# Kernel tuning notes

Hardware: AMD Instinct MI355X
Metric: run time of the kernel (lower is better)

The kernel has to match this reference:

```python
import jax, jax.numpy as jnp
import numpy as np

B, N, C = 16, 1024, 1152
H = 16
D = C // H  # 72
INNER = 4608
EPS = 1e-6


def _layernorm(x, g, b):
    mu = jnp.mean(x, axis=-1, keepdims=True)
    var = jnp.mean(jnp.square(x - mu), axis=-1, keepdims=True)
    return (x - mu) * jax.lax.rsqrt(var + EPS) * g + b


def setup_inputs() -> dict:
    key = jax.random.key(0)
    ks = jax.random.split(key, 16)
    s_c = 1.0 / np.sqrt(C)
    s_i = 1.0 / np.sqrt(INNER)
    return {
        "x": jax.random.normal(ks[0], (B, N, C), dtype=jnp.float32),
        "ln1_g": jnp.ones((C,), jnp.float32),
        "ln1_b": jnp.zeros((C,), jnp.float32),
        # weights stored (in, out) so y = x @ W + b (equiv to torch x @ W.T + b)
        "qkv_w": jax.random.normal(ks[1], (C, 3 * C), jnp.float32) * s_c,
        "qkv_b": jnp.zeros((3 * C,), jnp.float32),
        "proj_w": jax.random.normal(ks[2], (C, C), jnp.float32) * s_c,
        "proj_b": jnp.zeros((C,), jnp.float32),
        "ln2_g": jnp.ones((C,), jnp.float32),
        "ln2_b": jnp.zeros((C,), jnp.float32),
        "fc1_w": jax.random.normal(ks[3], (C, INNER), jnp.float32) * s_c,
        "fc1_b": jnp.zeros((INNER,), jnp.float32),
        "fc2_w": jax.random.normal(ks[4], (INNER, C), jnp.float32) * s_i,
        "fc2_b": jnp.zeros((C,), jnp.float32),
    }


def reference(x, ln1_g, ln1_b, qkv_w, qkv_b, proj_w, proj_b,
              ln2_g, ln2_b, fc1_w, fc1_b, fc2_w, fc2_b):
    scale = D ** -0.5
    # --- attention branch ---
    h = _layernorm(x, ln1_g, ln1_b)
    qkv = (h @ qkv_w + qkv_b).reshape(B, N, 3, H, D)
    q, k, v = jnp.moveaxis(qkv, 2, 0)            # each (B, N, H, D)
    q = q.transpose(0, 2, 1, 3)                   # (B, H, N, D)
    k = k.transpose(0, 2, 1, 3)
    v = v.transpose(0, 2, 1, 3)
    attn = jnp.einsum('bhnd,bhmd->bhnm', q, k) * scale
    attn = jax.nn.softmax(attn, axis=-1)
    out = jnp.einsum('bhnm,bhmd->bhnd', attn, v)
    out = out.transpose(0, 2, 1, 3).reshape(B, N, C)
    x = x + out @ proj_w + proj_b
    # --- MLP branch ---
    h = _layernorm(x, ln2_g, ln2_b)
    h = jax.nn.gelu(h @ fc1_w + fc1_b, approximate=False)
    x = x + h @ fc2_w + fc2_b
    return x
```

## Files before the change

kernel.cpp:

```cpp
#include <hip/hip_runtime.h>
#include <hip/hip_bf16.h>

typedef unsigned short ushort_t;
using short8 = __attribute__((ext_vector_type(8))) short;
using f32x4  = __attribute__((ext_vector_type(4))) float;

#define DEVI __device__ __forceinline__

DEVI ushort_t f2bf(float f) {
    union { float f; unsigned u; } c; c.f = f;
    unsigned u = c.u;
    return (ushort_t)((u + 0x7FFF + ((u >> 16) & 1)) >> 16);
}

DEVI f32x4 mfma16(short8 a, short8 b, f32x4 c) {
    return __builtin_amdgcn_mfma_f32_16x16x32_bf16(a, b, c, 0, 0, 0);
}

DEVI void gld16(const void* g, void* l) {
    __builtin_amdgcn_global_load_lds(
        (const __attribute__((address_space(1))) unsigned int*)g,
        (__attribute__((address_space(3))) unsigned int*)l, 16, 0, 0);
}

#define Bsz 16
#define Ntok 1024
#define Cdim 1152
#define Hn 16
#define Dh 72
#define Dp 96
#define INNER 4608
#define Mrows (Bsz * Ntok)

#define OFF_QKV_WT  ((size_t)0)
#define OFF_PROJ_WT ((size_t)8257536)
#define OFF_FC1_WT  ((size_t)11206656)
#define OFF_FC2_WT  ((size_t)21823488)
#define OFF_H       ((size_t)33619968)
#define OFF_ATT     ((size_t)71368704)
#define OFF_Q       ((size_t)109117440)
#define OFF_K       ((size_t)159449088)
#define OFF_VT      ((size_t)209780736)
#define OFF_HIDDEN  OFF_Q

__global__ __launch_bounds__(256) void transpose_cast(
    const float* __restrict__ W, ushort_t* __restrict__ Wt, int K, int N)
{
    __shared__ float t[64][65];
    const int n0 = blockIdx.x * 64;
    const int k0 = blockIdx.y * 64;
    #pragma unroll
    for (int j = 0; j < 4; ++j) {
        int idx = threadIdx.x + j * 256;
        int r = idx >> 4;
        int c4 = idx & 15;
        float4 v = *(const float4*)&W[(size_t)(k0 + r) * N + n0 + c4 * 4];
        t[r][c4 * 4 + 0] = v.x; t[r][c4 * 4 + 1] = v.y;
        t[r][c4 * 4 + 2] = v.z; t[r][c4 * 4 + 3] = v.w;
    }
    __syncthreads();
    #pragma unroll
    for (int j = 0; j < 4; ++j) {
        int idx = threadIdx.x + j * 256;
        int rn = idx >> 4;
        int c4 = idx & 15;
        ushort4 o;
        o.x = f2bf(t[c4 * 4 + 0][rn]);
        o.y = f2bf(t[c4 * 4 + 1][rn]);
        o.z = f2bf(t[c4 * 4 + 2][rn]);
        o.w = f2bf(t[c4 * 4 + 3][rn]);
        *(ushort4*)&Wt[(size_t)(n0 + rn) * K + k0 + c4 * 4] = o;
    }
}

__global__ __launch_bounds__(256) void ln_kernel(
    const float* __restrict__ x, const float* __restrict__ g,
    const float* __restrict__ b, ushort_t* __restrict__ out)
{
    const int row = blockIdx.x;
    const int tid = threadIdx.x;
    const int lane = tid & 63, wid = tid >> 6;
    const float* xr = x + (size_t)row * Cdim;

    float4 v0 = ((const float4*)xr)[tid];
    float4 v1 = {0, 0, 0, 0};
    if (tid < 32) v1 = ((const float4*)xr)[256 + tid];
    float s  = v0.x + v0.y + v0.z + v0.w + v1.x + v1.y + v1.z + v1.w;
    float s2 = v0.x*v0.x + v0.y*v0.y + v0.z*v0.z + v0.w*v0.w
             + v1.x*v1.x + v1.y*v1.y + v1.z*v1.z + v1.w*v1.w;
    #pragma unroll
    for (int off = 32; off >= 1; off >>= 1) {
        s  += __shfl_xor(s, off);
        s2 += __shfl_xor(s2, off);
    }
    __shared__ float red[8];
    if (lane == 0) { red[wid] = s; red[4 + wid] = s2; }
    __syncthreads();
    s  = red[0] + red[1] + red[2] + red[3];
    s2 = red[4] + red[5] + red[6] + red[7];
    const float mu = s * (1.0f / Cdim);
    const float var = s2 * (1.0f / Cdim) - mu * mu;
    const float rs = rsqrtf(var + 1e-6f);

    ushort_t* orow = out + (size_t)row * Cdim;
    {
        float4 g4 = ((const float4*)g)[tid];
        float4 b4 = ((const float4*)b)[tid];
        ushort4 o;
        o.x = f2bf((v0.x - mu) * rs * g4.x + b4.x);
        o.y = f2bf((v0.y - mu) * rs * g4.y + b4.y);
        o.z = f2bf((v0.z - mu) * rs * g4.z + b4.z);
        o.w = f2bf((v0.w - mu) * rs * g4.w + b4.w);
        ((ushort4*)orow)[tid] = o;
    }
    if (tid < 32) {
        float4 g4 = ((const float4*)g)[256 + tid];
        float4 b4 = ((const float4*)b)[256 + tid];
        ushort4 o;
        o.x = f2bf((v1.x - mu) * rs * g4.x + b4.x);
        o.y = f2bf((v1.y - mu) * rs * g4.y + b4.y);
        o.z = f2bf((v1.z - mu) * rs * g4.z + b4.z);
        o.w = f2bf((v1.w - mu) * rs * g4.w + b4.w);
        ((ushort4*)orow)[256 + tid] = o;
    }
}

enum { EPI_QKV = 0, EPI_PROJ = 1, EPI_FC1 = 2, EPI_FC2 = 3 };

#define TBM 256
#define TBN 256
#define TBK 64
#define BUFB 65536

template<int EPI, int N, int K>
__global__ __launch_bounds__(512, 2) void gemm_bt(
    const ushort_t* __restrict__ A, const ushort_t* __restrict__ Bt,
    const float* __restrict__ bias, const float* __restrict__ resid,
    float* __restrict__ outf, ushort_t* __restrict__ outb,
    ushort_t* __restrict__ outq, ushort_t* __restrict__ outk, ushort_t* __restrict__ outv)
{
    __shared__ ushort_t smem[2 * BUFB / 2];
    const int tid = threadIdx.x;
    const int lane = tid & 63, wid = tid >> 6;
    const int wr = wid >> 2, wc = wid & 3;
    const int fr = lane & 15, fq = lane >> 4;
    const int m0 = blockIdx.y * TBM;
    const int n0 = blockIdx.x * TBN;

    const ushort_t* Ag = A + (size_t)m0 * K;
    const ushort_t* Bg = Bt + (size_t)n0 * K;

    size_t srcA[4], srcB[4]; int dstA[4], dstB[4];
    #pragma unroll
    for (int r = 0; r < 4; ++r) {
        const int chunk = r * 512 + tid;
        const int row = chunk >> 3;
        const int slot = chunk & 7;
        srcA[r] = (size_t)row * K + (slot ^ (row & 7)) * 8;
        srcB[r] = srcA[r];
        dstA[r] = (r * 512 + wid * 64) * 16;
        dstB[r] = 32768 + dstA[r];
    }

    auto STAGE = [&](int buf, int kk) {
        char* lb = (char*)smem + (size_t)buf * BUFB;
        #pragma unroll
        for (int r = 0; r < 4; ++r) gld16(Ag + srcA[r] + kk, lb + dstA[r]);
        #pragma unroll
        for (int r = 0; r < 4; ++r) gld16(Bg + srcB[r] + kk, lb + dstB[r]);
    };

    const int swz = (fr & 7) << 4;
    int aoff[8][2], boff[4][2];
    #pragma unroll
    for (int kh = 0; kh < 2; ++kh) {
        const int colb = (kh * 64 + fq * 16) ^ swz;
        #pragma unroll
        for (int i = 0; i < 8; ++i)
            aoff[i][kh] = (wr * 128 + i * 16 + fr) * 128 + colb;
        #pragma unroll
        for (int i = 0; i < 4; ++i)
            boff[i][kh] = 32768 + (wc * 64 + i * 16 + fr) * 128 + colb;
    }

    f32x4 acc[8][4] = {};
    const int NT = K / TBK;

    auto COMPUTE = [&](int t) {
        const char* lb = (const char*)smem + (size_t)(t & 1) * BUFB;
        #pragma unroll
        for (int kh = 0; kh < 2; ++kh) {
            short8 a[8], b[4];
            #pragma unroll
            for (int i = 0; i < 8; ++i) a[i] = *(const short8*)(lb + aoff[i][kh]);
            #pragma unroll
            for (int i = 0; i < 4; ++i) b[i] = *(const short8*)(lb + boff[i][kh]);
            __builtin_amdgcn_s_setprio(1);
            #pragma unroll
            for (int mi = 0; mi < 8; ++mi)
                #pragma unroll
                for (int ni = 0; ni < 4; ++ni)
                    acc[mi][ni] = mfma16(a[mi], b[ni], acc[mi][ni]);
            __builtin_amdgcn_s_setprio(0);
        }
    };

    STAGE(0, 0);
    for (int t = 0; t < NT; ++t) {
        if (t + 1 < NT) {
            STAGE((t + 1) & 1, (t + 1) * TBK);
            asm volatile("s_waitcnt vmcnt(8)" ::: "memory");
        } else {
            asm volatile("s_waitcnt vmcnt(0)" ::: "memory");
        }
        __builtin_amdgcn_s_barrier();
        __builtin_amdgcn_sched_barrier(0);
        COMPUTE(t);
        if (t + 1 < NT) __builtin_amdgcn_s_barrier();
    }

    #pragma unroll
    for (int mi = 0; mi < 8; ++mi) {
        #pragma unroll
        for (int ni = 0; ni < 4; ++ni) {
            const int col = n0 + wc * 64 + ni * 16 + fr;
            if (col < N) {
                const int rbase = m0 + wr * 128 + mi * 16 + fq * 4;
                #pragma unroll
                for (int i = 0; i < 4; ++i) {
                    const int r = rbase + i;
                    float v = acc[mi][ni][i];
                    if (EPI == EPI_QKV) {
                        v += bias[col];
                        const int which = col / Cdim;
                        const int rc = col % Cdim;
                        const int h = rc / Dh, d = rc % Dh;
                        const int b = r >> 10, n = r & 1023;
                        const size_t head = (size_t)(b * Hn + h);
                        if (which == 0)      outq[(head * Ntok + n) * Dp + d] = f2bf(v);
                        else if (which == 1) outk[(head * Ntok + n) * Dp + d] = f2bf(v);
                        else                 outv[(head * Dp + d) * Ntok + n] = f2bf(v);
                    } else if (EPI == EPI_PROJ) {
                        v += bias[col] + resid[(size_t)r * N + col];
                        outf[(size_t)r * N + col] = v;
                    } else if (EPI == EPI_FC1) {
                        v += bias[col];
                        v = 0.5f * v * (1.0f + erff(v * 0.70710678118f));
                        outb[(size_t)r * N + col] = f2bf(v);
                    } else {
                        v += bias[col] + outf[(size_t)r * N + col];
                        outf[(size_t)r * N + col] = v;
                    }
                }
            }
        }
    }
}

__global__ __launch_bounds__(256) void attn_kernel(
    const ushort_t* __restrict__ q, const ushort_t* __restrict__ k,
    const ushort_t* __restrict__ vt, ushort_t* __restrict__ out)
{
    const int tid = threadIdx.x;
    const int lane = tid & 63, wid = tid >> 6;
    const int bh = blockIdx.y;
    const int qbase = blockIdx.x * 128 + wid * 32;
    const int fr = lane & 15, fq = lane >> 4;
    const ushort_t* qh = q  + (size_t)bh * Ntok * Dp;
    const ushort_t* kh = k  + (size_t)bh * Ntok * Dp;
    const ushort_t* vh = vt + (size_t)bh * Dp * Ntok;

    short8 aq[2][3];
    #pragma unroll
    for (int t = 0; t < 2; ++t)
        #pragma unroll
        for (int ks = 0; ks < 3; ++ks)
            aq[t][ks] = *(const short8*)&qh[(size_t)(qbase + t * 16 + fr) * Dp + ks * 32 + fq * 8];

    f32x4 o[2][5] = {};
    float mrun[2][4], lsum[2][4];
    #pragma unroll
    for (int t = 0; t < 2; ++t)
        #pragma unroll
        for (int i = 0; i < 4; ++i) { mrun[t][i] = -1e30f; lsum[t][i] = 0.0f; }

    __shared__ ushort_t plds[4][2][16][32];
    const float scale = 0.117851130f;

    for (int kv = 0; kv < Ntok; kv += 32) {
        short8 kb0[3], kb1[3], bv[5];
        #pragma unroll
        for (int ks = 0; ks < 3; ++ks) {
            kb0[ks] = *(const short8*)&kh[(size_t)(kv + fr) * Dp + ks * 32 + fq * 8];
            kb1[ks] = *(const short8*)&kh[(size_t)(kv + 16 + fr) * Dp + ks * 32 + fq * 8];
        }
        #pragma unroll
        for (int dt = 0; dt < 5; ++dt)
            bv[dt] = *(const short8*)&vh[(size_t)(dt * 16 + fr) * Ntok + kv + fq * 8];

        f32x4 s[2][2] = {};
        __builtin_amdgcn_s_setprio(1);
        #pragma unroll
        for (int ks = 0; ks < 3; ++ks)
            #pragma unroll
            for (int t = 0; t < 2; ++t) {
                s[t][0] = mfma16(aq[t][ks], kb0[ks], s[t][0]);
                s[t][1] = mfma16(aq[t][ks], kb1[ks], s[t][1]);
            }
        __builtin_amdgcn_s_setprio(0);

        #pragma unroll
        for (int t = 0; t < 2; ++t) {
            float a0[4], a1[4];
            float lmax = -1e30f;
            #pragma unroll
            for (int i = 0; i < 4; ++i) {
                a0[i] = s[t][0][i] * scale;
                a1[i] = s[t][1][i] * scale;
                lmax = fmaxf(lmax, fmaxf(a0[i], a1[i]));
            }
            const float mmin = fminf(fminf(mrun[t][0], mrun[t][1]),
                                     fminf(mrun[t][2], mrun[t][3]));
            if (!__all(lmax <= mmin + 8.0f)) {
                #pragma unroll
                for (int i = 0; i < 4; ++i) {
                    float mx = fmaxf(a0[i], a1[i]);
                    mx = fmaxf(mx, __shfl_xor(mx, 1));
                    mx = fmaxf(mx, __shfl_xor(mx, 2));
                    mx = fmaxf(mx, __shfl_xor(mx, 4));
                    mx = fmaxf(mx, __shfl_xor(mx, 8));
                    const float mnew = fmaxf(mrun[t][i], mx);
                    const float f = __expf(mrun[t][i] - mnew);
                    mrun[t][i] = mnew;
                    lsum[t][i] *= f;
                    #pragma unroll
                    for (int dt = 0; dt < 5; ++dt) o[t][dt][i] *= f;
                }
            }
            #pragma unroll
            for (int i = 0; i < 4; ++i) {
                float p0 = __expf(a0[i] - mrun[t][i]);
                float p1 = __expf(a1[i] - mrun[t][i]);
                lsum[t][i] += p0 + p1;
                plds[wid][t][fq * 4 + i][fr]      = f2bf(p0);
                plds[wid][t][fq * 4 + i][16 + fr] = f2bf(p1);
            }
        }
        short8 pa[2];
        #pragma unroll
        for (int t = 0; t < 2; ++t)
            pa[t] = *(const short8*)&plds[wid][t][fr][fq * 8];
        __builtin_amdgcn_s_setprio(1);
        #pragma unroll
        for (int dt = 0; dt < 5; ++dt)
            #pragma unroll
            for (int t = 0; t < 2; ++t)
                o[t][dt] = mfma16(pa[t], bv[dt], o[t][dt]);
        __builtin_amdgcn_s_setprio(0);
    }

    const int b = bh >> 4, h = bh & 15;
    #pragma unroll
    for (int t = 0; t < 2; ++t) {
        float inv[4];
        #pragma unroll
        for (int i = 0; i < 4; ++i) {
            float s = lsum[t][i];
            s += __shfl_xor(s, 1);
            s += __shfl_xor(s, 2);
            s += __shfl_xor(s, 4);
            s += __shfl_xor(s, 8);
            inv[i] = 1.0f / s;
        }
        #pragma unroll
        for (int dt = 0; dt < 5; ++dt) {
            const int d = dt * 16 + fr;
            if (d < Dh) {
                #pragma unroll
                for (int i = 0; i < 4; ++i) {
                    const size_t idx = ((size_t)(b * Ntok) + qbase + t * 16 + fq * 4 + i) * Cdim + h * Dh + d;
                    out[idx] = f2bf(o[t][dt][i] * inv[i]);
                }
            }
        }
    }
}

extern "C" void kernel_launch(void* const* d_in, const int* in_sizes, int n_in,
                              void* d_out, int out_size, void* d_ws, size_t ws_size,
                              hipStream_t stream) {
    const float* x      = (const float*)d_in[0];
    const float* ln1_g  = (const float*)d_in[1];
    const float* ln1_b  = (const float*)d_in[2];
    const float* qkv_w  = (const float*)d_in[3];
    const float* qkv_b  = (const float*)d_in[4];
    const float* proj_w = (const float*)d_in[5];
    const float* proj_b = (const float*)d_in[6];
    const float* ln2_g  = (const float*)d_in[7];
    const float* ln2_b  = (const float*)d_in[8];
    const float* fc1_w  = (const float*)d_in[9];
    const float* fc1_b  = (const float*)d_in[10];
    const float* fc2_w  = (const float*)d_in[11];
    const float* fc2_b  = (const float*)d_in[12];

    char* ws = (char*)d_ws;
    ushort_t* qkv_wT  = (ushort_t*)(ws + OFF_QKV_WT);
    ushort_t* proj_wT = (ushort_t*)(ws + OFF_PROJ_WT);
    ushort_t* fc1_wT  = (ushort_t*)(ws + OFF_FC1_WT);
    ushort_t* fc2_wT  = (ushort_t*)(ws + OFF_FC2_WT);
    ushort_t* hbuf    = (ushort_t*)(ws + OFF_H);
    ushort_t* attnout = (ushort_t*)(ws + OFF_ATT);
    ushort_t* qb      = (ushort_t*)(ws + OFF_Q);
    ushort_t* kb      = (ushort_t*)(ws + OFF_K);
    ushort_t* vtb     = (ushort_t*)(ws + OFF_VT);
    ushort_t* hidden  = (ushort_t*)(ws + OFF_HIDDEN);
    float* out = (float*)d_out;

    hipMemsetAsync(ws + OFF_Q, 0, (size_t)3 * 50331648, stream);

    transpose_cast<<<dim3(3 * Cdim / 64, Cdim / 64), 256, 0, stream>>>(qkv_w, qkv_wT, Cdim, 3 * Cdim);
    transpose_cast<<<dim3(Cdim / 64, Cdim / 64), 256, 0, stream>>>(proj_w, proj_wT, Cdim, Cdim);
    transpose_cast<<<dim3(INNER / 64, Cdim / 64), 256, 0, stream>>>(fc1_w, fc1_wT, Cdim, INNER);
    transpose_cast<<<dim3(Cdim / 64, INNER / 64), 256, 0, stream>>>(fc2_w, fc2_wT, INNER, Cdim);

    ln_kernel<<<Mrows, 256, 0, stream>>>(x, ln1_g, ln1_b, hbuf);

    gemm_bt<EPI_QKV, 3 * Cdim, Cdim><<<dim3(14, Mrows / TBM), 512, 0, stream>>>(
        hbuf, qkv_wT, qkv_b, nullptr, nullptr, nullptr, qb, kb, vtb);

    attn_kernel<<<dim3(Ntok / 128, Bsz * Hn), 256, 0, stream>>>(qb, kb, vtb, attnout);

    gemm_bt<EPI_PROJ, Cdim, Cdim><<<dim3(5, Mrows / TBM), 512, 0, stream>>>(
        attnout, proj_wT, proj_b, x, out, nullptr, nullptr, nullptr, nullptr);

    ln_kernel<<<Mrows, 256, 0, stream>>>(out, ln2_g, ln2_b, hbuf);

    gemm_bt<EPI_FC1, INNER, Cdim><<<dim3(18, Mrows / TBM), 512, 0, stream>>>(
        hbuf, fc1_wT, fc1_b, nullptr, nullptr, hidden, nullptr, nullptr, nullptr);

    gemm_bt<EPI_FC2, Cdim, INNER><<<dim3(5, Mrows / TBM), 512, 0, stream>>>(
        hidden, fc2_wT, fc2_b, nullptr, out, nullptr, nullptr, nullptr, nullptr);
}
```

Baseline: 1.221 ms.

## Interleave GEMM tile loads with MFMA phases in a finer-grained pipeline

Restructures the bf16 GEMM main loop. Each k-tile is now split into four compute quarters, and the global-to-LDS loads for the next tile are spread across those quarters, with per-quarter waitcnt and barrier points. B fragments are loaded once per tile and reused, and A fragments are read two row-blocks at a time. The aim is to overlap memory traffic with MFMA work more evenly, which cuts register pressure from holding all A fragments. The cost is many more barriers per tile, and the waitcnt and barrier choreography is delicate.

```diff
diff --git a/kernel.cpp b/kernel.cpp
--- a/kernel.cpp
+++ b/kernel.cpp
@@ -129,8 +129,6 @@
 
 #define TBM 256
 #define TBN 256
-#define TBK 64
-#define BUFB 65536
 
 template<int EPI, int N, int K>
 __global__ __launch_bounds__(512, 2) void gemm_bt(
@@ -139,7 +137,7 @@
     float* __restrict__ outf, ushort_t* __restrict__ outb,
     ushort_t* __restrict__ outq, ushort_t* __restrict__ outk, ushort_t* __restrict__ outv)
 {
-    __shared__ ushort_t smem[2 * BUFB / 2];
+    __shared__ ushort_t smem[65536];
     const int tid = threadIdx.x;
     const int lane = tid & 63, wid = tid >> 6;
     const int wr = wid >> 2, wc = wid & 3;
@@ -150,73 +148,83 @@
     const ushort_t* Ag = A + (size_t)m0 * K;
     const ushort_t* Bg = Bt + (size_t)n0 * K;
 
-    size_t srcA[4], srcB[4]; int dstA[4], dstB[4];
-    #pragma unroll
-    for (int r = 0; r < 4; ++r) {
-        const int chunk = r * 512 + tid;
-        const int row = chunk >> 3;
-        const int slot = chunk & 7;
-        srcA[r] = (size_t)row * K + (slot ^ (row & 7)) * 8;
-        srcB[r] = srcA[r];
-        dstA[r] = (r * 512 + wid * 64) * 16;
-        dstB[r] = 32768 + dstA[r];
-    }
-
-    auto STAGE = [&](int buf, int kk) {
-        char* lb = (char*)smem + (size_t)buf * BUFB;
-        #pragma unroll
-        for (int r = 0; r < 4; ++r) gld16(Ag + srcA[r] + kk, lb + dstA[r]);
-        #pragma unroll
-        for (int r = 0; r < 4; ++r) gld16(Bg + srcB[r] + kk, lb + dstB[r]);
+    const int l3 = lane >> 3, l7 = lane & 7;
+    const int srow = wid * 8 + l3;
+    const size_t sOff = (size_t)srow * K + (size_t)((l7 ^ l3) * 8);
+    char* sm = (char*)smem;
+
+    auto stA = [&](int buf, int rowbase, int kk) {
+        gld16(Ag + (size_t)rowbase * K + sOff + kk,
+              sm + buf * 65536 + rowbase * 128 + wid * 1024);
     };
-
-    const int swz = (fr & 7) << 4;
-    int aoff[8][2], boff[4][2];
-    #pragma unroll
-    for (int kh = 0; kh < 2; ++kh) {
-        const int colb = (kh * 64 + fq * 16) ^ swz;
-        #pragma unroll
-        for (int i = 0; i < 8; ++i)
-            aoff[i][kh] = (wr * 128 + i * 16 + fr) * 128 + colb;
-        #pragma unroll
-        for (int i = 0; i < 4; ++i)
-            boff[i][kh] = 32768 + (wc * 64 + i * 16 + fr) * 128 + colb;
-    }
+    auto stB = [&](int buf, int rowbase, int kk) {
+        gld16(Bg + (size_t)rowbase * K + sOff + kk,
+              sm + buf * 65536 + 32768 + rowbase * 128 + wid * 1024);
+    };
+
+    const int sw0 = (fq ^ l7) * 16;
+    const int sw1 = ((4 + fq) ^ l7) * 16;
+    const int baseA = wr * 16384 + fr * 128;
+    const int baseB = 32768 + wc * 8192 + fr * 128;
 
     f32x4 acc[8][4] = {};
-    const int NT = K / TBK;
-
-    auto COMPUTE = [&](int t) {
-        const char* lb = (const char*)smem + (size_t)(t & 1) * BUFB;
-        #pragma unroll
-        for (int kh = 0; kh < 2; ++kh) {
-            short8 a[8], b[4];
-            #pragma unroll
-            for (int i = 0; i < 8; ++i) a[i] = *(const short8*)(lb + aoff[i][kh]);
-            #pragma unroll
-            for (int i = 0; i < 4; ++i) b[i] = *(const short8*)(lb + boff[i][kh]);
+    short8 b[4][2];
+    const int NT = K / 64;
+
+    stB(0, 0, 0);   stB(0, 64, 0);
+    stB(0, 128, 0); stB(0, 192, 0);
+    stA(0, 0, 0);   stA(0, 128, 0);
+    stA(0, 64, 0);  stA(0, 192, 0);
+    asm volatile("s_waitcnt vmcnt(2)" ::: "memory");
+    __builtin_amdgcn_s_barrier();
+    __builtin_amdgcn_sched_barrier(0);
+
+    for (int t = 0; t < NT; ++t) {
+        const int cur = t & 1, nxt = cur ^ 1;
+        const int kk = (t + 1) * 64;
+        const char* lb = sm + cur * 65536;
+        const bool more = (t + 1 < NT);
+        #pragma unroll
+        for (int q = 0; q < 4; ++q) {
+            short8 a[2][2];
+            a[0][0] = *(const short8*)(lb + baseA + (2 * q) * 2048 + sw0);
+            a[0][1] = *(const short8*)(lb + baseA + (2 * q) * 2048 + sw1);
+            a[1][0] = *(const short8*)(lb + baseA + (2 * q + 1) * 2048 + sw0);
+            a[1][1] = *(const short8*)(lb + baseA + (2 * q + 1) * 2048 + sw1);
+            if (q == 0) {
+                #pragma unroll
+                for (int ni = 0; ni < 4; ++ni) {
+                    b[ni][0] = *(const short8*)(lb + baseB + ni * 2048 + sw0);
+                    b[ni][1] = *(const short8*)(lb + baseB + ni * 2048 + sw1);
+                }
+            }
+            if (more) {
+                if (q == 0) { stB(nxt, 0, kk);   stB(nxt, 64, kk); }
+                if (q == 1) { stB(nxt, 128, kk); stB(nxt, 192, kk); }
+                if (q == 2) { stA(nxt, 0, kk);   stA(nxt, 128, kk); }
+                if (q == 3) { stA(nxt, 64, kk);  stA(nxt, 192, kk); }
+            }
+            if (q == 1) {
+                if (more) { asm volatile("s_waitcnt vmcnt(4)" ::: "memory"); }
+                else      { asm volatile("s_waitcnt vmcnt(0)" ::: "memory"); }
+            }
+            if (q == 3 && more) { asm volatile("s_waitcnt vmcnt(2)" ::: "memory"); }
+            __builtin_amdgcn_sched_barrier(0);
+            __builtin_amdgcn_s_barrier();
+            __builtin_amdgcn_sched_barrier(0);
             __builtin_amdgcn_s_setprio(1);
             #pragma unroll
-            for (int mi = 0; mi < 8; ++mi)
+            for (int j = 0; j < 2; ++j)
                 #pragma unroll
                 for (int ni = 0; ni < 4; ++ni)
-                    acc[mi][ni] = mfma16(a[mi], b[ni], acc[mi][ni]);
+                    #pragma unroll
+                    for (int kh = 0; kh < 2; ++kh)
+                        acc[2 * q + j][ni] = mfma16(a[j][kh], b[ni][kh], acc[2 * q + j][ni]);
             __builtin_amdgcn_s_setprio(0);
-        }
-    };
-
-    STAGE(0, 0);
-    for (int t = 0; t < NT; ++t) {
-        if (t + 1 < NT) {
-            STAGE((t + 1) & 1, (t + 1) * TBK);
-            asm volatile("s_waitcnt vmcnt(8)" ::: "memory");
-        } else {
-            asm volatile("s_waitcnt vmcnt(0)" ::: "memory");
-        }
-        __builtin_amdgcn_s_barrier();
-        __builtin_amdgcn_sched_barrier(0);
-        COMPUTE(t);
-        if (t + 1 < NT) __builtin_amdgcn_s_barrier();
+            __builtin_amdgcn_sched_barrier(0);
+            __builtin_amdgcn_s_barrier();
+            __builtin_amdgcn_sched_barrier(0);
+        }
     }
 
     #pragma unroll
@@ -235,8 +243,8 @@
                         const int which = col / Cdim;
                         const int rc = col % Cdim;
                         const int h = rc / Dh, d = rc % Dh;
-                        const int b = r >> 10, n = r & 1023;
-                        const size_t head = (size_t)(b * Hn + h);
+                        const int b2 = r >> 10, n = r & 1023;
+                        const size_t head = (size_t)(b2 * Hn + h);
                         if (which == 0)      outq[(head * Ntok + n) * Dp + d] = f2bf(v);
                         else if (which == 1) outk[(head * Ntok + n) * Dp + d] = f2bf(v);
                         else                 outv[(head * Dp + d) * Ntok + n] = f2bf(v);
```

After: 1.186 ms. -2.9%, faster.

## Restructure GEMM mainloop into 4-stage K=32 pipeline with split A/B staging

Applied to the files above, without the earlier changes.

Replaces the double-buffered K=64 GEMM mainloop with a four-buffer K=32 pipeline that prefetches two tiles ahead. A and B loads are issued separately, each interleaved with one half of the MFMA work, and a new XOR swizzle suits the 64-byte rows. The goal is to hide global-to-LDS latency and spread memory traffic across the compute phases. The cost is more barriers per K step, and the LDS footprint stays at 128 KB.

```diff
diff --git a/kernel.cpp b/kernel.cpp
--- a/kernel.cpp
+++ b/kernel.cpp
@@ -129,8 +129,6 @@
 
 #define TBM 256
 #define TBN 256
-#define TBK 64
-#define BUFB 65536
 
 template<int EPI, int N, int K>
 __global__ __launch_bounds__(512, 2) void gemm_bt(
@@ -139,7 +137,7 @@
     float* __restrict__ outf, ushort_t* __restrict__ outb,
     ushort_t* __restrict__ outq, ushort_t* __restrict__ outk, ushort_t* __restrict__ outv)
 {
-    __shared__ ushort_t smem[2 * BUFB / 2];
+    __shared__ ushort_t smem[4 * 16384];
     const int tid = threadIdx.x;
     const int lane = tid & 63, wid = tid >> 6;
     const int wr = wid >> 2, wc = wid & 3;
@@ -150,73 +148,84 @@
     const ushort_t* Ag = A + (size_t)m0 * K;
     const ushort_t* Bg = Bt + (size_t)n0 * K;
 
-    size_t srcA[4], srcB[4]; int dstA[4], dstB[4];
-    #pragma unroll
-    for (int r = 0; r < 4; ++r) {
-        const int chunk = r * 512 + tid;
-        const int row = chunk >> 3;
-        const int slot = chunk & 7;
-        srcA[r] = (size_t)row * K + (slot ^ (row & 7)) * 8;
-        srcB[r] = srcA[r];
-        dstA[r] = (r * 512 + wid * 64) * 16;
-        dstB[r] = 32768 + dstA[r];
-    }
-
-    auto STAGE = [&](int buf, int kk) {
-        char* lb = (char*)smem + (size_t)buf * BUFB;
-        #pragma unroll
-        for (int r = 0; r < 4; ++r) gld16(Ag + srcA[r] + kk, lb + dstA[r]);
-        #pragma unroll
-        for (int r = 0; r < 4; ++r) gld16(Bg + srcB[r] + kk, lb + dstB[r]);
+    const int srow = tid >> 2;
+    const int fsrc = (srow & 3) ^ ((srow >> 2) & 3);
+    const size_t sOff = (size_t)srow * K + (size_t)(((tid & 3) ^ fsrc) * 8);
+    char* sm = (char*)smem;
+
+    auto stage_A = [&](int buf, int kk) {
+        char* lb = sm + buf * 32768;
+        gld16(Ag + sOff + kk, lb + tid * 16);
+        gld16(Ag + (size_t)128 * K + sOff + kk, lb + 8192 + tid * 16);
     };
-
-    const int swz = (fr & 7) << 4;
-    int aoff[8][2], boff[4][2];
-    #pragma unroll
-    for (int kh = 0; kh < 2; ++kh) {
-        const int colb = (kh * 64 + fq * 16) ^ swz;
-        #pragma unroll
-        for (int i = 0; i < 8; ++i)
-            aoff[i][kh] = (wr * 128 + i * 16 + fr) * 128 + colb;
-        #pragma unroll
-        for (int i = 0; i < 4; ++i)
-            boff[i][kh] = 32768 + (wc * 64 + i * 16 + fr) * 128 + colb;
-    }
+    auto stage_B = [&](int buf, int kk) {
+        char* lb = sm + buf * 32768;
+        gld16(Bg + sOff + kk, lb + 16384 + tid * 16);
+        gld16(Bg + (size_t)128 * K + sOff + kk, lb + 24576 + tid * 16);
+    };
+
+    const int rslot = (fq ^ (fr & 3) ^ ((fr >> 2) & 3)) * 16;
+    int aoff[8], boff[4];
+    #pragma unroll
+    for (int i = 0; i < 8; ++i) aoff[i] = (wr * 128 + i * 16 + fr) * 64 + rslot;
+    #pragma unroll
+    for (int i = 0; i < 4; ++i) boff[i] = 16384 + (wc * 64 + i * 16 + fr) * 64 + rslot;
 
     f32x4 acc[8][4] = {};
-    const int NT = K / TBK;
-
-    auto COMPUTE = [&](int t) {
-        const char* lb = (const char*)smem + (size_t)(t & 1) * BUFB;
-        #pragma unroll
-        for (int kh = 0; kh < 2; ++kh) {
-            short8 a[8], b[4];
-            #pragma unroll
-            for (int i = 0; i < 8; ++i) a[i] = *(const short8*)(lb + aoff[i][kh]);
-            #pragma unroll
-            for (int i = 0; i < 4; ++i) b[i] = *(const short8*)(lb + boff[i][kh]);
-            __builtin_amdgcn_s_setprio(1);
-            #pragma unroll
-            for (int mi = 0; mi < 8; ++mi)
-                #pragma unroll
-                for (int ni = 0; ni < 4; ++ni)
-                    acc[mi][ni] = mfma16(a[mi], b[ni], acc[mi][ni]);
-            __builtin_amdgcn_s_setprio(0);
-        }
-    };
-
-    STAGE(0, 0);
+    const int NT = K / 32;
+
+    stage_A(0, 0);  stage_B(0, 0);
+    stage_A(1, 32); stage_B(1, 32);
+    asm volatile("s_waitcnt vmcnt(4)" ::: "memory");
+    __builtin_amdgcn_s_barrier();
+    __builtin_amdgcn_sched_barrier(0);
+
     for (int t = 0; t < NT; ++t) {
+        const char* lb = sm + (t & 3) * 32768;
+        const int kk = (t + 2) * 32;
+        const bool pf = (t + 2) < NT;
+        const int nbuf = (t + 2) & 3;
+
+        short8 b[4], a[4];
+        #pragma unroll
+        for (int i = 0; i < 4; ++i) b[i] = *(const short8*)(lb + boff[i]);
+        #pragma unroll
+        for (int i = 0; i < 4; ++i) a[i] = *(const short8*)(lb + aoff[i]);
+        if (pf) stage_A(nbuf, kk);
+        __builtin_amdgcn_sched_barrier(0);
+        __builtin_amdgcn_s_barrier();
+        __builtin_amdgcn_sched_barrier(0);
+        __builtin_amdgcn_s_setprio(1);
+        #pragma unroll
+        for (int mi = 0; mi < 4; ++mi)
+            #pragma unroll
+            for (int ni = 0; ni < 4; ++ni)
+                acc[mi][ni] = mfma16(a[mi], b[ni], acc[mi][ni]);
+        __builtin_amdgcn_s_setprio(0);
+        __builtin_amdgcn_sched_barrier(0);
+        __builtin_amdgcn_s_barrier();
+        __builtin_amdgcn_sched_barrier(0);
+
+        #pragma unroll
+        for (int i = 0; i < 4; ++i) a[i] = *(const short8*)(lb + aoff[4 + i]);
+        if (pf) stage_B(nbuf, kk);
         if (t + 1 < NT) {
-            STAGE((t + 1) & 1, (t + 1) * TBK);
-            asm volatile("s_waitcnt vmcnt(8)" ::: "memory");
-        } else {
-            asm volatile("s_waitcnt vmcnt(0)" ::: "memory");
-        }
+            if (pf) { asm volatile("s_waitcnt vmcnt(4)" ::: "memory"); }
+            else    { asm volatile("s_waitcnt vmcnt(0)" ::: "memory"); }
+        }
+        __builtin_amdgcn_sched_barrier(0);
         __builtin_amdgcn_s_barrier();
         __builtin_amdgcn_sched_barrier(0);
-        COMPUTE(t);
-        if (t + 1 < NT) __builtin_amdgcn_s_barrier();
+        __builtin_amdgcn_s_setprio(1);
+        #pragma unroll
+        for (int mi = 0; mi < 4; ++mi)
+            #pragma unroll
+            for (int ni = 0; ni < 4; ++ni)
+                acc[4 + mi][ni] = mfma16(a[mi], b[ni], acc[4 + mi][ni]);
+        __builtin_amdgcn_s_setprio(0);
+        __builtin_amdgcn_sched_barrier(0);
+        __builtin_amdgcn_s_barrier();
+        __builtin_amdgcn_sched_barrier(0);
     }
 
     #pragma unroll
@@ -235,8 +244,8 @@
                         const int which = col / Cdim;
                         const int rc = col % Cdim;
                         const int h = rc / Dh, d = rc % Dh;
-                        const int b = r >> 10, n = r & 1023;
-                        const size_t head = (size_t)(b * Hn + h);
+                        const int b2 = r >> 10, n = r & 1023;
+                        const size_t head = (size_t)(b2 * Hn + h);
                         if (which == 0)      outq[(head * Ntok + n) * Dp + d] = f2bf(v);
                         else if (which == 1) outk[(head * Ntok + n) * Dp + d] = f2bf(v);
                         else                 outv[(head * Dp + d) * Ntok + n] = f2bf(v);
```

After: 1.221 ms. No clear change (+0.0%).
